# Kernel tuning notes

Measured on AMD Instinct MI355X. Metric: run time of the kernel, lower is better.

Reference implementation:

```python
import jax, jax.numpy as jnp
import numpy as np

DN = ('NCDHW', 'OIDHW', 'NCDHW')
HEAD_COUNT = 8
LN_EPS = 1e-5


def _dwpw(x, dw_w, dw_b, pw_w, pw_b):
    # depthwise 3x3x3 conv (groups=C) followed by pointwise 1x1x1 conv, both with bias
    cin = x.shape[1]
    y = jax.lax.conv_general_dilated(x, dw_w, (1, 1, 1), [(1, 1), (1, 1), (1, 1)],
                                     dimension_numbers=DN, feature_group_count=cin)
    y = y + dw_b[None, :, None, None, None]
    y = jax.lax.conv_general_dilated(y, pw_w, (1, 1, 1), [(0, 0), (0, 0), (0, 0)],
                                     dimension_numbers=DN)
    return y + pw_b[None, :, None, None, None]


def setup_inputs() -> dict:
    key = jax.random.key(0)
    ks = iter(jax.random.split(key, 64))
    C, KC, VC = 256, 256, 256
    n, t, h, w = 4, 16, 28, 28
    d = {}
    d['input_rgb'] = jax.random.normal(next(ks), (n, C, t, h, w), dtype=jnp.float32)
    d['input_flow'] = jax.random.normal(next(ks), (n, C, t, h, w), dtype=jnp.float32)

    def conv_params(cin, cout, pfx):
        d[pfx + '_dw_w'] = jax.random.normal(next(ks), (cin, 1, 3, 3, 3), dtype=jnp.float32) * 0.05
        d[pfx + '_dw_b'] = jnp.zeros((cin,), dtype=jnp.float32)
        d[pfx + '_pw_w'] = jax.random.normal(next(ks), (cout, cin, 1, 1, 1), dtype=jnp.float32) * 0.05
        d[pfx + '_pw_b'] = jnp.zeros((cout,), dtype=jnp.float32)

    for s in ('rgb', 'flow'):
        for p, cout in (('k', KC), ('q', KC), ('v', VC)):
            conv_params(C, cout, f'{s}_{p}')
    conv_params(2 * VC, 2 * C, 'rp')
    return d


def reference(input_rgb, input_flow,
              rgb_k_dw_w, rgb_k_dw_b, rgb_k_pw_w, rgb_k_pw_b,
              rgb_q_dw_w, rgb_q_dw_b, rgb_q_pw_w, rgb_q_pw_b,
              rgb_v_dw_w, rgb_v_dw_b, rgb_v_pw_w, rgb_v_pw_b,
              flow_k_dw_w, flow_k_dw_b, flow_k_pw_w, flow_k_pw_b,
              flow_q_dw_w, flow_q_dw_b, flow_q_pw_w, flow_q_pw_b,
              flow_v_dw_w, flow_v_dw_b, flow_v_pw_w, flow_v_pw_b,
              rp_dw_w, rp_dw_b, rp_pw_w, rp_pw_b):
    n, C, t, h, w = input_rgb.shape
    S = t * h * w
    fused = jnp.concatenate([input_rgb, input_flow], axis=1)  # [n, 2C, t, h, w]

    def proj(x, dw_w, dw_b, pw_w, pw_b):
        return _dwpw(x, dw_w, dw_b, pw_w, pw_b).reshape(n, -1, S)

    keys = jnp.concatenate([proj(input_rgb, rgb_k_dw_w, rgb_k_dw_b, rgb_k_pw_w, rgb_k_pw_b),
                            proj(input_flow, flow_k_dw_w, flow_k_dw_b, flow_k_pw_w, flow_k_pw_b)], axis=1)
    queries = jnp.concatenate([proj(input_rgb, rgb_q_dw_w, rgb_q_dw_b, rgb_q_pw_w, rgb_q_pw_b),
                               proj(input_flow, flow_q_dw_w, flow_q_dw_b, flow_q_pw_w, flow_q_pw_b)], axis=1)
    values = jnp.concatenate([proj(input_rgb, rgb_v_dw_w, rgb_v_dw_b, rgb_v_pw_w, rgb_v_pw_b),
                              proj(input_flow, flow_v_dw_w, flow_v_dw_b, flow_v_pw_w, flow_v_pw_b)], axis=1)

    H = HEAD_COUNT
    hk = keys.shape[1] // H
    hv = values.shape[1] // H
    K = jax.nn.softmax(keys.reshape(n, H, hk, S), axis=3)      # softmax over sequence
    Q = jax.nn.softmax(queries.reshape(n, H, hk, S), axis=2)   # softmax over head channels
    V = values.reshape(n, H, hv, S)

    ctx = jnp.einsum('nhks,nhvs->nhkv', K, V)                   # [n,H,hk,hv]
    att = jnp.einsum('nhkv,nhks->nhvs', ctx, Q)                 # [n,H,hv,S]
    aggregated = att.reshape(n, H * hv, t, h, w)                # [n, 2*VC, t, h, w]

    rep = _dwpw(aggregated, rp_dw_w, rp_dw_b, rp_pw_w, rp_pw_b)
    x = rep + fused
    # f.layer_norm(x, x.size()): normalize over the ENTIRE tensor, no affine
    m = x.mean()
    v = x.var()
    return (x - m) / jnp.sqrt(v + LN_EPS)
```

## Files before the change

kernel.cpp:

```cpp
#include <hip/hip_runtime.h>
#include <math.h>


constexpr int NN = 4;
constexpr int C1 = 256;
constexpr int C2 = 512;
constexpr int TT = 16;
constexpr int SP = TT * 28 * 28;
constexpr long long NB = (long long)NN * C2 * SP;
constexpr int HEADS = 8;
constexpr int CTX_CHUNKS = 7;
constexpr int SBLKS = 98;
constexpr int STATS_PARTS = SBLKS * 4 * 4;
constexpr double TOTAL_ELEMS = (double)NB;

typedef __attribute__((ext_vector_type(8))) short bf16x8;
typedef __attribute__((ext_vector_type(4))) short bf16x4;
typedef __attribute__((ext_vector_type(4))) float f32x4;

__device__ __forceinline__ short f2bf(float f)
{
    unsigned u = __float_as_uint(f);
    unsigned r = u + 0x7FFFu + ((u >> 16) & 1u);
    return (short)(r >> 16);
}
__device__ __forceinline__ float bf2f(short s)
{
    return __uint_as_float(((unsigned)(unsigned short)s) << 16);
}

__device__ __forceinline__ float4 loadvec4(const float* p)
{
    return *(const float4*)p;
}
__device__ __forceinline__ float4 loadvec4(const short* p)
{
    bf16x4 v = *(const bf16x4*)p;
    return (float4){bf2f(v[0]), bf2f(v[1]), bf2f(v[2]), bf2f(v[3])};
}

__device__ __forceinline__ void gload16(const short* g, short* l)
{
    __builtin_amdgcn_global_load_lds(
        (const __attribute__((address_space(1))) unsigned int*)g,
        (__attribute__((address_space(3))) unsigned int*)l,
        16, 0, 0);
}

__global__ __launch_bounds__(256)
void wcvt_kernel(const float* __restrict__ w0, const float* __restrict__ w1,
                 const float* __restrict__ w2, const float* __restrict__ w3,
                 const float* __restrict__ w4, const float* __restrict__ w5,
                 const float* __restrict__ w6, short* __restrict__ out)
{
    int i = blockIdx.x * 256 + threadIdx.x;
    if (i >= 655360) return;
    const float* src; int off;
    if (i < 393216) {
        int seg = i >> 16; off = i & 65535;
        src = seg == 0 ? w0 : seg == 1 ? w1 : seg == 2 ? w2
            : seg == 3 ? w3 : seg == 4 ? w4 : w5;
    } else { src = w6; off = i - 393216; }
    out[i] = f2bf(src[off]);
}

template<typename IT, int NSET>
__global__ __launch_bounds__(256)
void dwv_kernel(const IT* __restrict__ in,
                const float* __restrict__ w0c, const float* __restrict__ b0c,
                short* __restrict__ o0,
                const float* __restrict__ w1c, const float* __restrict__ b1c,
                short* __restrict__ o1,
                const float* __restrict__ w2c, const float* __restrict__ b2c,
                short* __restrict__ o2, int Cin)
{
    const int split = blockIdx.x, c = blockIdx.y, n = blockIdx.z;
    const int t0 = split * 8, t1 = t0 + 8;
    const int zs = (t0 - 1 > 0) ? t0 - 1 : 0;
    const int ze = (t1 < 15) ? t1 : 15;
    __shared__ float tile[2][900];
    const int tid = threadIdx.x;
    const size_t ibase = ((size_t)(n * Cin + c)) * TT * 784;
    const IT* inp = in + ibase;

    const float* wp[3] = {w0c, w1c, w2c};
    const float* bp[3] = {b0c, b1c, b2c};
    short* op[3] = {o0, o1, o2};
    float w[NSET][27], bv[NSET];
#pragma unroll
    for (int g = 0; g < NSET; ++g) {
#pragma unroll
        for (int i = 0; i < 27; ++i) w[g][i] = wp[g][c * 27 + i];
        bv[g] = bp[g][c];
    }

    for (int i = tid; i < 1800; i += 256) ((float*)tile)[i] = 0.f;

    const bool act = tid < 196;
    const int pos = tid * 4;
    const int hh = pos / 28, ww = pos - hh * 28;
    const int ladr = (hh + 1) * 30 + ww + 1;
    const int rbase = hh * 30 + ww;

    float4 preg = {0.f, 0.f, 0.f, 0.f};
    if (act) preg = loadvec4(inp + (size_t)zs * 784 + pos);

    float a0[NSET][4], a1[NSET][4], a2[NSET][4];
#pragma unroll
    for (int g = 0; g < NSET; ++g)
#pragma unroll
        for (int k = 0; k < 4; ++k) { a0[g][k] = bv[g]; a1[g][k] = bv[g]; a2[g][k] = bv[g]; }

    for (int z = zs; z <= ze; ++z) {
        float* tb = tile[z & 1];
        __syncthreads();
        if (act) {
            tb[ladr] = preg.x; tb[ladr + 1] = preg.y;
            tb[ladr + 2] = preg.z; tb[ladr + 3] = preg.w;
            if (z < ze) preg = loadvec4(inp + (size_t)(z + 1) * 784 + pos);
        }
        __syncthreads();
        if (act) {
            float v[3][6];
#pragma unroll
            for (int r = 0; r < 3; ++r)
#pragma unroll
                for (int j = 0; j < 6; ++j)
                    v[r][j] = tb[rbase + r * 30 + j];
#pragma unroll
            for (int g = 0; g < NSET; ++g)
#pragma unroll
                for (int dh = 0; dh < 3; ++dh)
#pragma unroll
                    for (int dw = 0; dw < 3; ++dw) {
                        const float wa = w[g][18 + dh * 3 + dw];
                        const float wb = w[g][9 + dh * 3 + dw];
                        const float wc2 = w[g][dh * 3 + dw];
#pragma unroll
                        for (int k = 0; k < 4; ++k) {
                            const float val = v[dh][k + dw];
                            a0[g][k] += val * wa;
                            a1[g][k] += val * wb;
                            a2[g][k] += val * wc2;
                        }
                    }
            if (z - 1 >= t0) {
#pragma unroll
                for (int g = 0; g < NSET; ++g) {
                    bf16x4 pk;
#pragma unroll
                    for (int k = 0; k < 4; ++k) pk[k] = f2bf(a0[g][k]);
                    *(bf16x4*)&op[g][ibase + (size_t)(z - 1) * 784 + pos] = pk;
                }
            }
#pragma unroll
            for (int g = 0; g < NSET; ++g)
#pragma unroll
                for (int k = 0; k < 4; ++k) {
                    a0[g][k] = a1[g][k]; a1[g][k] = a2[g][k]; a2[g][k] = bv[g];
                }
        }
    }
    if (act && ze >= t0 && ze < t1) {
#pragma unroll
        for (int g = 0; g < NSET; ++g) {
            bf16x4 pk;
#pragma unroll
            for (int k = 0; k < 4; ++k) pk[k] = f2bf(a0[g][k]);
            *(bf16x4*)&op[g][ibase + (size_t)ze * 784 + pos] = pk;
        }
    }
}

template<int MODE>
__global__ __launch_bounds__(256)
void pw_mfma_kernel(const short* __restrict__ WbA, const float* __restrict__ biasA,
                    const short* __restrict__ actA, short* __restrict__ outA,
                    const short* __restrict__ WbV, const float* __restrict__ biasV,
                    const short* __restrict__ actV, short* __restrict__ outV,
                    const float* __restrict__ rgb, const float* __restrict__ flow,
                    double* __restrict__ partials, float2* __restrict__ kpart,
                    int Cin, size_t nStride, size_t cStride, int chOff)
{
    __shared__ short smem[34816];
    const int tid = threadIdx.x;
    const int w = tid >> 6, lane = tid & 63;
    int s0, m0, n, seg = 0, sBlk;
    if constexpr (MODE == 2) {
        const int b = blockIdx.x;
        const int r = b & 7, t = b >> 3;
        const int mBlk = t & 3, q = t >> 2;
        const int g = q * 8 + r;
        n = g / SBLKS; sBlk = g % SBLKS;
        s0 = sBlk * 128; m0 = mBlk * 128;
    } else {
        sBlk = blockIdx.x; s0 = sBlk * 128; n = blockIdx.z;
        if constexpr (MODE == 0) { seg = blockIdx.y >> 1; m0 = (blockIdx.y & 1) * 128; }
        else m0 = blockIdx.y * 128;
    }
    const short* Wb = (MODE == 0 && seg) ? WbV : WbA;
    const float* bias = (MODE == 0 && seg) ? biasV : biasA;
    const short* actp = (MODE == 0 && seg) ? actV : actA;
    short* outB = (MODE == 0 && seg) ? outV : outA;

    const short* aSrc = Wb + (size_t)m0 * Cin;
    const short* bSrc = actp + (size_t)n * Cin * SP;
    f32x4 acc[4][4];
#pragma unroll
    for (int i = 0; i < 4; ++i)
#pragma unroll
        for (int j = 0; j < 4; ++j)
            acc[i][j] = (f32x4){0.f, 0.f, 0.f, 0.f};
    const int lrow = lane >> 3, lslot = lane & 7;
    const int wr = w >> 1, wc = w & 1;
    const int kg = tid >> 4, scb = tid & 15;
    const int nt = Cin >> 6;

    {
        short* nA = smem;
        short* nB = smem + 16384;
#pragma unroll
        for (int cc = 0; cc < 4; ++cc) {
            const int chunk = w * 4 + cc;
            const int row = chunk * 8 + lrow;
            const int ss = lslot ^ (row & 7);
            gload16(aSrc + (size_t)row * Cin + ss * 8, &nA[chunk * 512]);
        }
        bf16x8 breg[4];
#pragma unroll
        for (int r = 0; r < 4; ++r)
            breg[r] = *(const bf16x8*)(bSrc + (size_t)(kg * 4 + r) * SP + s0 + scb * 8);
#pragma unroll
        for (int j = 0; j < 8; ++j) {
            bf16x4 pk;
#pragma unroll
            for (int r = 0; r < 4; ++r) pk[r] = breg[r][j];
            const int srow = scb * 8 + j;
            const int slot = (kg >> 1) ^ (scb & 7);
            *(bf16x4*)&nB[srow * 72 + slot * 8 + (kg & 1) * 4] = pk;
        }
    }
    __syncthreads();

    for (int t = 0; t < nt; ++t) {
        short* cA = smem + (t & 1) * 8192;
        short* cB = smem + 16384 + (t & 1) * 9216;
        short* nA = smem + ((t + 1) & 1) * 8192;
        short* nB = smem + 16384 + ((t + 1) & 1) * 9216;
        const bool more = (t + 1) < nt;
        bf16x8 bnext[4];
        if (more) {
            const int kt = (t + 1) << 6;
#pragma unroll
            for (int cc = 0; cc < 4; ++cc) {
                const int chunk = w * 4 + cc;
                const int row = chunk * 8 + lrow;
                const int ss = lslot ^ (row & 7);
                gload16(aSrc + (size_t)row * Cin + kt + ss * 8, &nA[chunk * 512]);
            }
#pragma unroll
            for (int r = 0; r < 4; ++r)
                bnext[r] = *(const bf16x8*)(bSrc + (size_t)(kt + kg * 4 + r) * SP + s0 + scb * 8);
        }
#pragma unroll
        for (int kf = 0; kf < 2; ++kf) {
            bf16x8 af[4], bfr[4];
            const int kb = kf * 4 + (lane >> 4);
#pragma unroll
            for (int i = 0; i < 4; ++i) {
                const int row = wr * 64 + i * 16 + (lane & 15);
                af[i] = *(const bf16x8*)&cA[row * 64 + ((kb ^ (row & 7)) << 3)];
            }
#pragma unroll
            for (int j = 0; j < 4; ++j) {
                const int srow = wc * 64 + j * 16 + (lane & 15);
                bfr[j] = *(const bf16x8*)&cB[srow * 72 + ((kb ^ ((srow >> 3) & 7)) << 3)];
            }
#pragma unroll
            for (int i = 0; i < 4; ++i)
#pragma unroll
                for (int j = 0; j < 4; ++j)
                    acc[i][j] = __builtin_amdgcn_mfma_f32_16x16x32_bf16(
                        af[i], bfr[j], acc[i][j], 0, 0, 0);
        }
        if (more) {
#pragma unroll
            for (int j = 0; j < 8; ++j) {
                bf16x4 pk;
#pragma unroll
                for (int r = 0; r < 4; ++r) pk[r] = bnext[r][j];
                const int srow = scb * 8 + j;
                const int slot = (kg >> 1) ^ (scb & 7);
                *(bf16x4*)&nB[srow * 72 + slot * 8 + (kg & 1) * 4] = pk;
            }
        }
        __syncthreads();
    }

    if constexpr (MODE == 0) {
        short* ep = smem;
#pragma unroll
        for (int i = 0; i < 4; ++i) {
            const int mloc = wr * 64 + i * 16 + (lane >> 4) * 4;
#pragma unroll
            for (int j = 0; j < 4; ++j) {
                const int sloc = wc * 64 + j * 16 + (lane & 15);
#pragma unroll
                for (int r = 0; r < 4; ++r)
                    ep[(mloc + r) * 136 + sloc] =
                        f2bf(acc[i][j][r] + bias[m0 + mloc + r]);
            }
        }
        __syncthreads();
        short* op = outB + (size_t)n * nStride;
#pragma unroll
        for (int cc = 0; cc < 8; ++cc) {
            const int idx = tid + cc * 256;
            const int mloc = idx >> 4, ch = idx & 15;
            bf16x8 v = *(const bf16x8*)&ep[mloc * 136 + ch * 8];
            *(bf16x8*)&op[(size_t)(chOff + m0 + mloc) * cStride + s0 + ch * 8] = v;
        }
        if (seg == 0) {
            const int row = tid >> 1, half = tid & 1;
            const short* rp = &ep[row * 136 + half * 64];
            float mx = -1e30f;
#pragma unroll 8
            for (int j = 0; j < 64; ++j) mx = fmaxf(mx, bf2f(rp[j]));
            float sum = 0.f;
#pragma unroll 8
            for (int j = 0; j < 64; ++j) sum += __expf(bf2f(rp[j]) - mx);
            const float mo = __shfl_xor(mx, 1, 64);
            const float so = __shfl_xor(sum, 1, 64);
            const float mg = fmaxf(mx, mo);
            const float sg = sum * __expf(mx - mg) + so * __expf(mo - mg);
            if (half == 0)
                kpart[(size_t)(n * 512 + chOff + m0 + row) * SBLKS + sBlk] =
                    (float2){mg, sg};
        }
    } else if constexpr (MODE == 1) {
        short* ep = smem;
#pragma unroll
        for (int i = 0; i < 4; ++i) {
            const int mb = wr * 64 + i * 16 + (lane >> 4) * 4;
#pragma unroll
            for (int j = 0; j < 4; ++j) {
                const int sloc = wc * 64 + j * 16 + (lane & 15);
                bf16x4 pk;
#pragma unroll
                for (int r = 0; r < 4; ++r)
                    pk[r] = f2bf(acc[i][j][r] + bias[m0 + mb + r]);
                *(bf16x4*)&ep[sloc * 136 + mb] = pk;
            }
        }
        __syncthreads();
#pragma unroll
        for (int cc = 0; cc < 8; ++cc) {
            const int idx = tid + cc * 256;
            const int sloc = idx >> 4, ch = idx & 15;
            bf16x8 v = *(const bf16x8*)&ep[sloc * 136 + ch * 8];
            *(bf16x8*)&outA[((size_t)n * SP + s0 + sloc) * 512 + chOff + m0 + ch * 8] = v;
        }
    } else {
        float* ep = (float*)smem;
#pragma unroll
        for (int i = 0; i < 4; ++i) {
            const int mloc = wr * 64 + i * 16 + (lane >> 4) * 4;
#pragma unroll
            for (int j = 0; j < 4; ++j) {
                const int sloc = wc * 64 + j * 16 + (lane & 15);
#pragma unroll
                for (int r = 0; r < 4; ++r)
                    ep[(mloc + r) * 132 + sloc] =
                        acc[i][j][r] + bias[m0 + mloc + r];
            }
        }
        __syncthreads();
        short* xo = outA + (size_t)n * C2 * SP;
        const float* rbase = (m0 < 256)
            ? rgb + ((size_t)n * 256 + m0) * SP
            : flow + ((size_t)n * 256 + (m0 - 256)) * SP;
        double ls = 0.0, lss = 0.0;
#pragma unroll
        for (int cc = 0; cc < 8; ++cc) {
            const int idx = tid + cc * 256;
            const int mloc = idx >> 4, ch = idx & 15;
            float4 a0 = *(const float4*)&ep[mloc * 132 + ch * 8];
            float4 a1 = *(const float4*)&ep[mloc * 132 + ch * 8 + 4];
            float4 r0 = *(const float4*)&rbase[(size_t)mloc * SP + s0 + ch * 8];
            float4 r1 = *(const float4*)&rbase[(size_t)mloc * SP + s0 + ch * 8 + 4];
            bf16x8 pk;
            pk[0] = f2bf(a0.x + r0.x); pk[1] = f2bf(a0.y + r0.y);
            pk[2] = f2bf(a0.z + r0.z); pk[3] = f2bf(a0.w + r0.w);
            pk[4] = f2bf(a1.x + r1.x); pk[5] = f2bf(a1.y + r1.y);
            pk[6] = f2bf(a1.z + r1.z); pk[7] = f2bf(a1.w + r1.w);
            *(bf16x8*)&xo[(size_t)(m0 + mloc) * SP + s0 + ch * 8] = pk;
#pragma unroll
            for (int k = 0; k < 8; ++k) {
                const double xv = (double)bf2f(pk[k]);
                ls += xv; lss += xv * xv;
            }
        }
        __shared__ double s1[256], s2[256];
        s1[tid] = ls; s2[tid] = lss;
        __syncthreads();
        for (int st = 128; st > 0; st >>= 1) {
            if (tid < st) { s1[tid] += s1[tid + st]; s2[tid] += s2[tid + st]; }
            __syncthreads();
        }
        if (tid == 0) {
            partials[2 * blockIdx.x] = s1[0];
            partials[2 * blockIdx.x + 1] = s2[0];
        }
    }
}

__global__ __launch_bounds__(256)
void kstats_reduce_kernel(const float2* __restrict__ kpart, float2* __restrict__ st)
{
    const int row = blockIdx.x * 256 + threadIdx.x;
    const float2* p = kpart + (size_t)row * SBLKS;
    float m = -1e30f, s = 0.f;
    for (int b = 0; b < SBLKS; ++b) {
        float2 e = p[b];
        float nm = fmaxf(m, e.x);
        s = s * __expf(m - nm) + e.y * __expf(e.x - nm);
        m = nm;
    }
    st[row] = (float2){m, 1.f / s};
}

__global__ __launch_bounds__(256)
void ctx_mfma_kernel(const short* __restrict__ Kb, const short* __restrict__ Vb,
                     const float2* __restrict__ stats, float* __restrict__ part)
{
    const int chunk = blockIdx.x, nh = blockIdx.y;
    const short* Kp = Kb + (size_t)nh * 64 * SP;
    const short* Vp = Vb + (size_t)nh * 64 * SP;
    __shared__ short lK[64 * 256];
    __shared__ short lV[64 * 256];
    const int tid = threadIdx.x;
    const int w = tid >> 6, lane = tid & 63;
    const int wr = w >> 1, wc = w & 1;
    f32x4 acc[2][2];
#pragma unroll
    for (int i = 0; i < 2; ++i)
#pragma unroll
        for (int j = 0; j < 2; ++j)
            acc[i][j] = (f32x4){0.f, 0.f, 0.f, 0.f};

    float km8[8], ki8[8];
#pragma unroll
    for (int ps = 0; ps < 8; ++ps) {
        float2 s = stats[nh * 64 + (tid >> 5) + ps * 8];
        km8[ps] = s.x; ki8[ps] = s.y;
    }

    for (int sub = 0; sub < 7; ++sub) {
        const int sOff = chunk * 1792 + sub * 256;
#pragma unroll
        for (int cc = 0; cc < 8; ++cc) {
            const int ch = w * 8 + cc;
            const int row = ch * 2 + (lane >> 5);
            const int sc = lane & 31;
            gload16(Vp + (size_t)row * SP + sOff + ((sc ^ (row & 7)) << 3),
                    &lV[ch * 512]);
        }
#pragma unroll
        for (int ps = 0; ps < 8; ++ps) {
            const int row = (tid >> 5) + ps * 8;
            const int sc = tid & 31;
            bf16x8 kv = *(const bf16x8*)(Kp + (size_t)row * SP + sOff + sc * 8);
            bf16x8 ev;
#pragma unroll
            for (int j = 0; j < 8; ++j)
                ev[j] = f2bf(__expf(bf2f(kv[j]) - km8[ps]) * ki8[ps]);
            *(bf16x8*)&lK[row * 256 + ((sc ^ (row & 7)) << 3)] = ev;
        }
        __syncthreads();
#pragma unroll
        for (int ks = 0; ks < 8; ++ks) {
            const int kb = ks * 4 + (lane >> 4);
            bf16x8 ak[2], bv[2];
#pragma unroll
            for (int i = 0; i < 2; ++i) {
                const int rk = wr * 32 + i * 16 + (lane & 15);
                ak[i] = *(const bf16x8*)&lK[rk * 256 + ((kb ^ (rk & 7)) << 3)];
            }
#pragma unroll
            for (int j = 0; j < 2; ++j) {
                const int rv = wc * 32 + j * 16 + (lane & 15);
                bv[j] = *(const bf16x8*)&lV[rv * 256 + ((kb ^ (rv & 7)) << 3)];
            }
#pragma unroll
            for (int i = 0; i < 2; ++i)
#pragma unroll
                for (int j = 0; j < 2; ++j)
                    acc[i][j] = __builtin_amdgcn_mfma_f32_16x16x32_bf16(
                        ak[i], bv[j], acc[i][j], 0, 0, 0);
        }
        __syncthreads();
    }
    float* op = part + ((size_t)nh * CTX_CHUNKS + chunk) * 4096;
#pragma unroll
    for (int i = 0; i < 2; ++i)
#pragma unroll
        for (int j = 0; j < 2; ++j)
#pragma unroll
            for (int r = 0; r < 4; ++r) {
                const int k = wr * 32 + i * 16 + (lane >> 4) * 4 + r;
                const int v = wc * 32 + j * 16 + (lane & 15);
                op[k * 64 + v] = acc[i][j][r];
            }
}

__global__ __launch_bounds__(256)
void ctx_reduce_kernel(const float* __restrict__ part, float* __restrict__ ctx)
{
    const int nh = blockIdx.x;
    for (int e = threadIdx.x; e < 4096; e += 256) {
        float s = 0.f;
        for (int c = 0; c < CTX_CHUNKS; ++c)
            s += part[((size_t)nh * CTX_CHUNKS + c) * 4096 + e];
        ctx[(size_t)nh * 4096 + e] = s;
    }
}

__global__ __launch_bounds__(256)
void att_kernel(const float* __restrict__ ctx, const short* __restrict__ Qb,
                short* __restrict__ out)
{
    const int nh = blockIdx.y;
    const int n = nh >> 3, h = nh & 7;
    const int s0 = blockIdx.x * 64;
    const float* cp = ctx + (size_t)nh * 4096;
    __shared__ short lC[64 * 64];
    __shared__ short lQ[64 * 64];
    __shared__ float red[64][4];
    __shared__ short lO[64 * 72];
    const int tid = threadIdx.x;
    const int w = tid >> 6, lane = tid & 63;

#pragma unroll
    for (int u = 0; u < 2; ++u) {
        const int si = (tid >> 6) + u * 4;
        const int v = tid & 63;
        bf16x8 pk;
#pragma unroll
        for (int j = 0; j < 8; ++j) pk[j] = f2bf(cp[(si * 8 + j) * 64 + v]);
        *(bf16x8*)&lC[v * 64 + ((si ^ (v & 7)) << 3)] = pk;
    }
    const int sq = tid >> 2, qpart = tid & 3;
    const short* Qrow = Qb + ((size_t)n * SP + s0 + sq) * 512 + h * 64 + qpart * 16;
    bf16x8 q0 = *(const bf16x8*)(Qrow);
    bf16x8 q1 = *(const bf16x8*)(Qrow + 8);
    float e[16];
    float mx = -1e30f;
#pragma unroll
    for (int j = 0; j < 8; ++j) {
        e[j] = bf2f(q0[j]); e[8 + j] = bf2f(q1[j]);
        mx = fmaxf(mx, fmaxf(e[j], e[8 + j]));
    }
    red[sq][qpart] = mx;
    __syncthreads();
    mx = fmaxf(fmaxf(red[sq][0], red[sq][1]), fmaxf(red[sq][2], red[sq][3]));
    float sum = 0.f;
#pragma unroll
    for (int j = 0; j < 16; ++j) { e[j] = __expf(e[j] - mx); sum += e[j]; }
    __syncthreads();
    red[sq][qpart] = sum;
    __syncthreads();
    const float sinv = 1.f / (red[sq][0] + red[sq][1] + red[sq][2] + red[sq][3]);
    bf16x8 p0, p1;
#pragma unroll
    for (int j = 0; j < 8; ++j) {
        p0[j] = f2bf(e[j] * sinv);
        p1[j] = f2bf(e[8 + j] * sinv);
    }
    *(bf16x8*)&lQ[sq * 64 + (((qpart * 2) ^ (sq & 7)) << 3)] = p0;
    *(bf16x8*)&lQ[sq * 64 + (((qpart * 2 + 1) ^ (sq & 7)) << 3)] = p1;
    __syncthreads();

    f32x4 acc[4];
#pragma unroll
    for (int i = 0; i < 4; ++i) acc[i] = (f32x4){0.f, 0.f, 0.f, 0.f};
    const int srow = w * 16 + (lane & 15);
#pragma unroll
    for (int ks = 0; ks < 2; ++ks) {
        const int kb = ks * 4 + (lane >> 4);
        bf16x8 bq = *(const bf16x8*)&lQ[srow * 64 + ((kb ^ (srow & 7)) << 3)];
#pragma unroll
        for (int i = 0; i < 4; ++i) {
            const int vr = i * 16 + (lane & 15);
            bf16x8 av = *(const bf16x8*)&lC[vr * 64 + ((kb ^ (vr & 7)) << 3)];
            acc[i] = __builtin_amdgcn_mfma_f32_16x16x32_bf16(av, bq, acc[i], 0, 0, 0);
        }
    }
#pragma unroll
    for (int i = 0; i < 4; ++i)
#pragma unroll
        for (int r = 0; r < 4; ++r)
            lO[(i * 16 + (lane >> 4) * 4 + r) * 72 + w * 16 + (lane & 15)] =
                f2bf(acc[i][r]);
    __syncthreads();
    short* op = out + (size_t)nh * 64 * SP;
#pragma unroll
    for (int cc = 0; cc < 2; ++cc) {
        const int idx = tid + cc * 256;
        const int v = idx >> 3, ch = idx & 7;
        bf16x8 t = *(const bf16x8*)&lO[v * 72 + ch * 8];
        *(bf16x8*)&op[(size_t)v * SP + s0 + ch * 8] = t;
    }
}

__global__ __launch_bounds__(256)
void stats_final_kernel(const double* __restrict__ partials, float* __restrict__ mv)
{
    double ls = 0.0, lss = 0.0;
    for (int i = threadIdx.x; i < STATS_PARTS; i += 256) {
        ls += partials[2 * i];
        lss += partials[2 * i + 1];
    }
    __shared__ double s1[256], s2[256];
    const int tid = threadIdx.x;
    s1[tid] = ls; s2[tid] = lss;
    __syncthreads();
    for (int s = 128; s > 0; s >>= 1) {
        if (tid < s) { s1[tid] += s1[tid + s]; s2[tid] += s2[tid + s]; }
        __syncthreads();
    }
    if (tid == 0) {
        double mean = s1[0] / TOTAL_ELEMS;
        double var = s2[0] / TOTAL_ELEMS - mean * mean;
        mv[0] = (float)mean;
        mv[1] = (float)(1.0 / sqrt(var + 1e-5));
    }
}

__global__ __launch_bounds__(256)
void normalize_kernel(const short* __restrict__ xb, float* __restrict__ out,
                      const float* __restrict__ mv)
{
    const float mean = mv[0], inv = mv[1];
    size_t i = ((size_t)blockIdx.x * 256 + threadIdx.x) * 8;
    const size_t tot = (size_t)NB;
    const size_t step = (size_t)gridDim.x * 2048;
    for (; i < tot; i += step) {
        bf16x8 v = *(const bf16x8*)&xb[i];
        float4 a, b;
        a.x = (bf2f(v[0]) - mean) * inv; a.y = (bf2f(v[1]) - mean) * inv;
        a.z = (bf2f(v[2]) - mean) * inv; a.w = (bf2f(v[3]) - mean) * inv;
        b.x = (bf2f(v[4]) - mean) * inv; b.y = (bf2f(v[5]) - mean) * inv;
        b.z = (bf2f(v[6]) - mean) * inv; b.w = (bf2f(v[7]) - mean) * inv;
        *(float4*)&out[i] = a;
        *(float4*)&out[i + 4] = b;
    }
}

extern "C" void kernel_launch(void* const* d_in, const int* in_sizes, int n_in,
                              void* d_out, int out_size, void* d_ws, size_t ws_size,
                              hipStream_t stream)
{
    (void)in_sizes; (void)n_in; (void)out_size; (void)ws_size;
    const float* rgb = (const float*)d_in[0];
    const float* flow = (const float*)d_in[1];
    float* ws = (float*)d_ws;

    short* bufK = (short*)ws;
    short* bufQ = (short*)(ws + NB / 2);
    short* bufV = (short*)(ws + NB);
    short* actK = (short*)(ws + 3 * NB / 2);
    short* actQ = (short*)(ws + 7 * NB / 4);
    short* actV = (short*)(ws + 2 * NB);
    short* wB   = (short*)(ws + 9 * NB / 4);
    float2* rowStats = (float2*)(wB + 655360);
    float* ctxBuf = (float*)(rowStats + 2048);
    double* partials = (double*)(ctxBuf + 32 * 4096);
    float* mv = (float*)(partials + 2 * STATS_PARTS);
    float2* kpart = (float2*)(mv + 8);
    float* ctxPart = ws + 3 * NB / 2;
    short* rpDw = actK;
    short* xb = bufK;

    const size_t nsA = (size_t)C2 * SP, csA = SP;

    wcvt_kernel<<<2560, 256, 0, stream>>>(
        (const float*)d_in[4], (const float*)d_in[12], (const float*)d_in[16],
        (const float*)d_in[24], (const float*)d_in[8], (const float*)d_in[20],
        (const float*)d_in[28], wB);

    for (int st = 0; st < 2; ++st) {
        const float* src = st ? flow : rgb;
        const int kI = st ? 14 : 2, qI = st ? 18 : 6, vI = st ? 22 : 10;
        const int choff = st ? 256 : 0;
        dwv_kernel<float, 3><<<dim3(2, C1, NN), 256, 0, stream>>>(
            src,
            (const float*)d_in[kI], (const float*)d_in[kI + 1], actK,
            (const float*)d_in[qI], (const float*)d_in[qI + 1], actQ,
            (const float*)d_in[vI], (const float*)d_in[vI + 1], actV, C1);
        pw_mfma_kernel<0><<<dim3(SBLKS, 4, NN), 256, 0, stream>>>(
            wB + (size_t)(st ? 2 : 0) * 65536, (const float*)d_in[kI + 3], actK, bufK,
            wB + (size_t)(st ? 3 : 1) * 65536, (const float*)d_in[vI + 3], actV, bufV,
            nullptr, nullptr, nullptr, kpart, C1, nsA, csA, choff);
        pw_mfma_kernel<1><<<dim3(SBLKS, 2, NN), 256, 0, stream>>>(
            wB + (size_t)(st ? 5 : 4) * 65536, (const float*)d_in[qI + 3], actQ, bufQ,
            nullptr, nullptr, nullptr, nullptr,
            nullptr, nullptr, nullptr, nullptr, C1, 0, 0, choff);
    }

    kstats_reduce_kernel<<<8, 256, 0, stream>>>(kpart, rowStats);
    ctx_mfma_kernel<<<dim3(CTX_CHUNKS, NN * HEADS), 256, 0, stream>>>(
        bufK, bufV, rowStats, ctxPart);
    ctx_reduce_kernel<<<NN * HEADS, 256, 0, stream>>>(ctxPart, ctxBuf);
    att_kernel<<<dim3(SP / 64, NN * HEADS), 256, 0, stream>>>(
        ctxBuf, bufQ, bufV);

    dwv_kernel<short, 1><<<dim3(2, C2, NN), 256, 0, stream>>>(
        bufV, (const float*)d_in[26], (const float*)d_in[27], rpDw,
        nullptr, nullptr, nullptr, nullptr, nullptr, nullptr, C2);
    pw_mfma_kernel<2><<<STATS_PARTS, 256, 0, stream>>>(
        wB + 6 * 65536, (const float*)d_in[29], rpDw, xb,
        nullptr, nullptr, nullptr, nullptr,
        rgb, flow, partials, nullptr, C2, 0, 0, 0);

    stats_final_kernel<<<1, 256, 0, stream>>>(partials, mv);
    normalize_kernel<<<2048, 256, 0, stream>>>(xb, (float*)d_out, mv);
}
```

Baseline: 419.3 us.

## Widen pointwise MFMA GEMM tile to 256 spatial columns with single-buffered B

```diff
diff --git a/kernel.cpp b/kernel.cpp
--- a/kernel.cpp
+++ b/kernel.cpp
@@ -10,7 +10,7 @@
 constexpr long long NB = (long long)NN * C2 * SP;
 constexpr int HEADS = 8;
 constexpr int CTX_CHUNKS = 7;
-constexpr int SBLKS = 98;
+constexpr int SBLKS = 49;
 constexpr int STATS_PARTS = SBLKS * 4 * 4;
 constexpr double TOTAL_ELEMS = (double)NB;
 
@@ -183,18 +183,18 @@
                     int Cin, size_t nStride, size_t cStride, int chOff)
 {
     __shared__ short smem[34816];
+    short* Bs = smem + 16384;
     const int tid = threadIdx.x;
     const int w = tid >> 6, lane = tid & 63;
     int s0, m0, n, seg = 0, sBlk;
     if constexpr (MODE == 2) {
-        const int b = blockIdx.x;
-        const int r = b & 7, t = b >> 3;
-        const int mBlk = t & 3, q = t >> 2;
-        const int g = q * 8 + r;
-        n = g / SBLKS; sBlk = g % SBLKS;
-        s0 = sBlk * 128; m0 = mBlk * 128;
+        const int bid = blockIdx.x;
+        const int wgid = (bid & 7) * 98 + (bid >> 3);
+        const int panel = wgid >> 2, mBlk = wgid & 3;
+        n = panel / SBLKS; sBlk = panel % SBLKS;
+        s0 = sBlk * 256; m0 = mBlk * 128;
     } else {
-        sBlk = blockIdx.x; s0 = sBlk * 128; n = blockIdx.z;
+        sBlk = blockIdx.x; s0 = sBlk * 256; n = blockIdx.z;
         if constexpr (MODE == 0) { seg = blockIdx.y >> 1; m0 = (blockIdx.y & 1) * 128; }
         else m0 = blockIdx.y * 128;
     }
@@ -205,199 +205,228 @@
 
     const short* aSrc = Wb + (size_t)m0 * Cin;
     const short* bSrc = actp + (size_t)n * Cin * SP;
-    f32x4 acc[4][4];
+    f32x4 acc[4][8];
 #pragma unroll
     for (int i = 0; i < 4; ++i)
 #pragma unroll
-        for (int j = 0; j < 4; ++j)
+        for (int j = 0; j < 8; ++j)
             acc[i][j] = (f32x4){0.f, 0.f, 0.f, 0.f};
     const int lrow = lane >> 3, lslot = lane & 7;
     const int wr = w >> 1, wc = w & 1;
     const int kg = tid >> 4, scb = tid & 15;
     const int nt = Cin >> 6;
 
-    {
-        short* nA = smem;
-        short* nB = smem + 16384;
-#pragma unroll
-        for (int cc = 0; cc < 4; ++cc) {
-            const int chunk = w * 4 + cc;
-            const int row = chunk * 8 + lrow;
-            const int ss = lslot ^ (row & 7);
-            gload16(aSrc + (size_t)row * Cin + ss * 8, &nA[chunk * 512]);
-        }
-        bf16x8 breg[4];
-#pragma unroll
-        for (int r = 0; r < 4; ++r)
-            breg[r] = *(const bf16x8*)(bSrc + (size_t)(kg * 4 + r) * SP + s0 + scb * 8);
+    bf16x8 breg[8];
+#pragma unroll
+    for (int cc = 0; cc < 4; ++cc) {
+        const int chunk = w * 4 + cc;
+        const int row = chunk * 8 + lrow;
+        const int ss = lslot ^ (row & 7);
+        gload16(aSrc + (size_t)row * Cin + ss * 8, &smem[chunk * 512]);
+    }
+#pragma unroll
+    for (int r = 0; r < 4; ++r)
+#pragma unroll
+        for (int h = 0; h < 2; ++h)
+            breg[r * 2 + h] = *(const bf16x8*)(bSrc + (size_t)(kg * 4 + r) * SP
+                                               + s0 + scb * 16 + h * 8);
+#pragma unroll
+    for (int h = 0; h < 2; ++h)
 #pragma unroll
         for (int j = 0; j < 8; ++j) {
             bf16x4 pk;
 #pragma unroll
-            for (int r = 0; r < 4; ++r) pk[r] = breg[r][j];
-            const int srow = scb * 8 + j;
+            for (int r = 0; r < 4; ++r) pk[r] = breg[r * 2 + h][j];
+            const int srow = scb * 16 + h * 8 + j;
             const int slot = (kg >> 1) ^ (scb & 7);
-            *(bf16x4*)&nB[srow * 72 + slot * 8 + (kg & 1) * 4] = pk;
-        }
-    }
+            *(bf16x4*)&Bs[srow * 72 + slot * 8 + (kg & 1) * 4] = pk;
+        }
     __syncthreads();
 
     for (int t = 0; t < nt; ++t) {
-        short* cA = smem + (t & 1) * 8192;
-        short* cB = smem + 16384 + (t & 1) * 9216;
-        short* nA = smem + ((t + 1) & 1) * 8192;
-        short* nB = smem + 16384 + ((t + 1) & 1) * 9216;
         const bool more = (t + 1) < nt;
-        bf16x8 bnext[4];
         if (more) {
             const int kt = (t + 1) << 6;
+            const int buf = (t + 1) & 1;
 #pragma unroll
             for (int cc = 0; cc < 4; ++cc) {
                 const int chunk = w * 4 + cc;
                 const int row = chunk * 8 + lrow;
                 const int ss = lslot ^ (row & 7);
-                gload16(aSrc + (size_t)row * Cin + kt + ss * 8, &nA[chunk * 512]);
+                gload16(aSrc + (size_t)row * Cin + kt + ss * 8,
+                        &smem[buf * 8192 + chunk * 512]);
             }
 #pragma unroll
             for (int r = 0; r < 4; ++r)
-                bnext[r] = *(const bf16x8*)(bSrc + (size_t)(kt + kg * 4 + r) * SP + s0 + scb * 8);
-        }
+#pragma unroll
+                for (int h = 0; h < 2; ++h)
+                    breg[r * 2 + h] = *(const bf16x8*)(bSrc + (size_t)(kt + kg * 4 + r) * SP
+                                                       + s0 + scb * 16 + h * 8);
+        }
+        const short* cA = smem + (t & 1) * 8192;
 #pragma unroll
         for (int kf = 0; kf < 2; ++kf) {
-            bf16x8 af[4], bfr[4];
             const int kb = kf * 4 + (lane >> 4);
+            bf16x8 af[4], bfr[8];
 #pragma unroll
             for (int i = 0; i < 4; ++i) {
                 const int row = wr * 64 + i * 16 + (lane & 15);
                 af[i] = *(const bf16x8*)&cA[row * 64 + ((kb ^ (row & 7)) << 3)];
             }
 #pragma unroll
-            for (int j = 0; j < 4; ++j) {
-                const int srow = wc * 64 + j * 16 + (lane & 15);
-                bfr[j] = *(const bf16x8*)&cB[srow * 72 + ((kb ^ ((srow >> 3) & 7)) << 3)];
+            for (int j = 0; j < 8; ++j) {
+                const int srow = wc * 128 + j * 16 + (lane & 15);
+                bfr[j] = *(const bf16x8*)&Bs[srow * 72 + ((kb ^ ((srow >> 4) & 7)) << 3)];
             }
 #pragma unroll
             for (int i = 0; i < 4; ++i)
 #pragma unroll
-                for (int j = 0; j < 4; ++j)
+                for (int j = 0; j < 8; ++j)
                     acc[i][j] = __builtin_amdgcn_mfma_f32_16x16x32_bf16(
                         af[i], bfr[j], acc[i][j], 0, 0, 0);
         }
+        __syncthreads();
         if (more) {
 #pragma unroll
-            for (int j = 0; j < 8; ++j) {
-                bf16x4 pk;
-#pragma unroll
-                for (int r = 0; r < 4; ++r) pk[r] = bnext[r][j];
-                const int srow = scb * 8 + j;
-                const int slot = (kg >> 1) ^ (scb & 7);
-                *(bf16x4*)&nB[srow * 72 + slot * 8 + (kg & 1) * 4] = pk;
-            }
+            for (int h = 0; h < 2; ++h)
+#pragma unroll
+                for (int j = 0; j < 8; ++j) {
+                    bf16x4 pk;
+#pragma unroll
+                    for (int r = 0; r < 4; ++r) pk[r] = breg[r * 2 + h][j];
+                    const int srow = scb * 16 + h * 8 + j;
+                    const int slot = (kg >> 1) ^ (scb & 7);
+                    *(bf16x4*)&Bs[srow * 72 + slot * 8 + (kg & 1) * 4] = pk;
+                }
         }
         __syncthreads();
     }
 
     if constexpr (MODE == 0) {
         short* ep = smem;
-#pragma unroll
-        for (int i = 0; i < 4; ++i) {
-            const int mloc = wr * 64 + i * 16 + (lane >> 4) * 4;
-#pragma unroll
-            for (int j = 0; j < 4; ++j) {
-                const int sloc = wc * 64 + j * 16 + (lane & 15);
-#pragma unroll
-                for (int r = 0; r < 4; ++r)
-                    ep[(mloc + r) * 136 + sloc] =
-                        f2bf(acc[i][j][r] + bias[m0 + mloc + r]);
-            }
-        }
-        __syncthreads();
-        short* op = outB + (size_t)n * nStride;
-#pragma unroll
-        for (int cc = 0; cc < 8; ++cc) {
-            const int idx = tid + cc * 256;
-            const int mloc = idx >> 4, ch = idx & 15;
-            bf16x8 v = *(const bf16x8*)&ep[mloc * 136 + ch * 8];
-            *(bf16x8*)&op[(size_t)(chOff + m0 + mloc) * cStride + s0 + ch * 8] = v;
-        }
-        if (seg == 0) {
-            const int row = tid >> 1, half = tid & 1;
-            const short* rp = &ep[row * 136 + half * 64];
-            float mx = -1e30f;
+        float mrun = -1e30f, srun = 0.f;
+#pragma unroll
+        for (int h = 0; h < 2; ++h) {
+            __syncthreads();
+            if (wc == h) {
+#pragma unroll
+                for (int i = 0; i < 4; ++i) {
+                    const int mloc = wr * 64 + i * 16 + (lane >> 4) * 4;
+#pragma unroll
+                    for (int j = 0; j < 8; ++j) {
+                        const int sloc = j * 16 + (lane & 15);
+#pragma unroll
+                        for (int r = 0; r < 4; ++r)
+                            ep[(mloc + r) * 136 + sloc] =
+                                f2bf(acc[i][j][r] + bias[m0 + mloc + r]);
+                    }
+                }
+            }
+            __syncthreads();
+            short* op = outB + (size_t)n * nStride;
+#pragma unroll
+            for (int cc = 0; cc < 8; ++cc) {
+                const int idx = tid + cc * 256;
+                const int mloc = idx >> 4, ch = idx & 15;
+                bf16x8 v = *(const bf16x8*)&ep[mloc * 136 + ch * 8];
+                *(bf16x8*)&op[(size_t)(chOff + m0 + mloc) * cStride
+                              + s0 + h * 128 + ch * 8] = v;
+            }
+            if (seg == 0) {
+                const int row = tid >> 1, half = tid & 1;
+                const short* rp = &ep[row * 136 + half * 64];
+                float mx = -1e30f;
 #pragma unroll 8
-            for (int j = 0; j < 64; ++j) mx = fmaxf(mx, bf2f(rp[j]));
-            float sum = 0.f;
+                for (int j = 0; j < 64; ++j) mx = fmaxf(mx, bf2f(rp[j]));
+                float sum = 0.f;
 #pragma unroll 8
-            for (int j = 0; j < 64; ++j) sum += __expf(bf2f(rp[j]) - mx);
-            const float mo = __shfl_xor(mx, 1, 64);
-            const float so = __shfl_xor(sum, 1, 64);
-            const float mg = fmaxf(mx, mo);
-            const float sg = sum * __expf(mx - mg) + so * __expf(mo - mg);
-            if (half == 0)
-                kpart[(size_t)(n * 512 + chOff + m0 + row) * SBLKS + sBlk] =
-                    (float2){mg, sg};
-        }
+                for (int j = 0; j < 64; ++j) sum += __expf(bf2f(rp[j]) - mx);
+                const float mo = __shfl_xor(mx, 1, 64);
+                const float so = __shfl_xor(sum, 1, 64);
+                const float mg = fmaxf(mx, mo);
+                const float sg = sum * __expf(mx - mg) + so * __expf(mo - mg);
+                const float nm = fmaxf(mrun, mg);
+                srun = srun * __expf(mrun - nm) + sg * __expf(mg - nm);
+                mrun = nm;
+            }
+        }
+        if (seg == 0 && (tid & 1) == 0)
+            kpart[(size_t)(n * 512 + chOff + m0 + (tid >> 1)) * SBLKS + sBlk] =
+                (float2){mrun, srun};
     } else if constexpr (MODE == 1) {
         short* ep = smem;
 #pragma unroll
-        for (int i = 0; i < 4; ++i) {
-            const int mb = wr * 64 + i * 16 + (lane >> 4) * 4;
-#pragma unroll
-            for (int j = 0; j < 4; ++j) {
-                const int sloc = wc * 64 + j * 16 + (lane & 15);
-                bf16x4 pk;
-#pragma unroll
-                for (int r = 0; r < 4; ++r)
-                    pk[r] = f2bf(acc[i][j][r] + bias[m0 + mb + r]);
-                *(bf16x4*)&ep[sloc * 136 + mb] = pk;
-            }
-        }
-        __syncthreads();
-#pragma unroll
-        for (int cc = 0; cc < 8; ++cc) {
-            const int idx = tid + cc * 256;
-            const int sloc = idx >> 4, ch = idx & 15;
-            bf16x8 v = *(const bf16x8*)&ep[sloc * 136 + ch * 8];
-            *(bf16x8*)&outA[((size_t)n * SP + s0 + sloc) * 512 + chOff + m0 + ch * 8] = v;
+        for (int h = 0; h < 2; ++h) {
+            __syncthreads();
+            if (wc == h) {
+#pragma unroll
+                for (int i = 0; i < 4; ++i) {
+                    const int mb = wr * 64 + i * 16 + (lane >> 4) * 4;
+#pragma unroll
+                    for (int j = 0; j < 8; ++j) {
+                        const int sloc = j * 16 + (lane & 15);
+                        bf16x4 pk;
+#pragma unroll
+                        for (int r = 0; r < 4; ++r)
+                            pk[r] = f2bf(acc[i][j][r] + bias[m0 + mb + r]);
+                        *(bf16x4*)&ep[sloc * 136 + mb] = pk;
+                    }
+                }
+            }
+            __syncthreads();
+#pragma unroll
+            for (int cc = 0; cc < 8; ++cc) {
+                const int idx = tid + cc * 256;
+                const int sloc = idx >> 4, ch = idx & 15;
+                bf16x8 v = *(const bf16x8*)&ep[sloc * 136 + ch * 8];
+                *(bf16x8*)&outA[((size_t)n * SP + s0 + h * 128 + sloc) * 512
+                                + chOff + m0 + ch * 8] = v;
+            }
         }
     } else {
         float* ep = (float*)smem;
-#pragma unroll
-        for (int i = 0; i < 4; ++i) {
-            const int mloc = wr * 64 + i * 16 + (lane >> 4) * 4;
-#pragma unroll
-            for (int j = 0; j < 4; ++j) {
-                const int sloc = wc * 64 + j * 16 + (lane & 15);
-#pragma unroll
-                for (int r = 0; r < 4; ++r)
-                    ep[(mloc + r) * 132 + sloc] =
-                        acc[i][j][r] + bias[m0 + mloc + r];
-            }
-        }
-        __syncthreads();
         short* xo = outA + (size_t)n * C2 * SP;
         const float* rbase = (m0 < 256)
             ? rgb + ((size_t)n * 256 + m0) * SP
             : flow + ((size_t)n * 256 + (m0 - 256)) * SP;
         double ls = 0.0, lss = 0.0;
 #pragma unroll
-        for (int cc = 0; cc < 8; ++cc) {
-            const int idx = tid + cc * 256;
-            const int mloc = idx >> 4, ch = idx & 15;
-            float4 a0 = *(const float4*)&ep[mloc * 132 + ch * 8];
-            float4 a1 = *(const float4*)&ep[mloc * 132 + ch * 8 + 4];
-            float4 r0 = *(const float4*)&rbase[(size_t)mloc * SP + s0 + ch * 8];
-            float4 r1 = *(const float4*)&rbase[(size_t)mloc * SP + s0 + ch * 8 + 4];
-            bf16x8 pk;
-            pk[0] = f2bf(a0.x + r0.x); pk[1] = f2bf(a0.y + r0.y);
-            pk[2] = f2bf(a0.z + r0.z); pk[3] = f2bf(a0.w + r0.w);
-            pk[4] = f2bf(a1.x + r1.x); pk[5] = f2bf(a1.y + r1.y);
-            pk[6] = f2bf(a1.z + r1.z); pk[7] = f2bf(a1.w + r1.w);
-            *(bf16x8*)&xo[(size_t)(m0 + mloc) * SP + s0 + ch * 8] = pk;
-#pragma unroll
-            for (int k = 0; k < 8; ++k) {
-                const double xv = (double)bf2f(pk[k]);
-                ls += xv; lss += xv * xv;
+        for (int h = 0; h < 2; ++h) {
+            __syncthreads();
+            if (wc == h) {
+#pragma unroll
+                for (int i = 0; i < 4; ++i) {
+                    const int mloc = wr * 64 + i * 16 + (lane >> 4) * 4;
+#pragma unroll
+                    for (int j = 0; j < 8; ++j) {
+                        const int sloc = j * 16 + (lane & 15);
+#pragma unroll
+                        for (int r = 0; r < 4; ++r)
+                            ep[(mloc + r) * 132 + sloc] =
+                                acc[i][j][r] + bias[m0 + mloc + r];
+                    }
+                }
+            }
+            __syncthreads();
+#pragma unroll
+            for (int cc = 0; cc < 8; ++cc) {
+                const int idx = tid + cc * 256;
+                const int mloc = idx >> 4, ch = idx & 15;
+                float4 a0 = *(const float4*)&ep[mloc * 132 + ch * 8];
+                float4 a1 = *(const float4*)&ep[mloc * 132 + ch * 8 + 4];
+                float4 r0 = *(const float4*)&rbase[(size_t)mloc * SP + s0 + h * 128 + ch * 8];
+                float4 r1 = *(const float4*)&rbase[(size_t)mloc * SP + s0 + h * 128 + ch * 8 + 4];
+                bf16x8 pk;
+                pk[0] = f2bf(a0.x + r0.x); pk[1] = f2bf(a0.y + r0.y);
+                pk[2] = f2bf(a0.z + r0.z); pk[3] = f2bf(a0.w + r0.w);
+                pk[4] = f2bf(a1.x + r1.x); pk[5] = f2bf(a1.y + r1.y);
+                pk[6] = f2bf(a1.z + r1.z); pk[7] = f2bf(a1.w + r1.w);
+                *(bf16x8*)&xo[(size_t)(m0 + mloc) * SP + s0 + h * 128 + ch * 8] = pk;
+#pragma unroll
+                for (int k = 0; k < 8; ++k) {
+                    const double xv = (double)bf2f(pk[k]);
+                    ls += xv; lss += xv * xv;
+                }
             }
         }
         __shared__ double s1[256], s2[256];
```

Measured after the change: 571.9 us. +36.4%, slower.
